# Performance work log

Measured on AMD Instinct MI355X. Metric: run time of the kernel, lower is better.

## Reference

```python
import jax, jax.numpy as jnp
import numpy as np

MODEL_DIM = 2048
HEAD_DIM = 64
STATE_DIM = 128
EXPAND = 2
CHUNK = 64
INNER = EXPAND * MODEL_DIM          # 4096
NHEADS = INNER // HEAD_DIM          # 64
IN_PROJ = INNER + 2 * STATE_DIM + NHEADS  # 4416
B_SZ = 2
SEQ = 4096


def segsum(x):
    """Stable segment sum: x (..., T) -> (..., T, T) with -inf above diagonal."""
    T = x.shape[-1]
    mask_strict = jnp.tril(jnp.ones((T, T), dtype=bool), -1)
    # element [d, e] = x[d] on strictly-lower triangle, 0 elsewhere
    xt = jnp.where(mask_strict, x[..., :, None], 0.0)
    seg = jnp.cumsum(xt, axis=-2)
    mask = jnp.tril(jnp.ones((T, T), dtype=bool), 0)
    return jnp.where(mask, seg, -jnp.inf)


def ssd(x, A, B, C, chunk):
    """Mamba-2 SSD. x:(b,L,h,p), A:(b,L,h), B/C:(b,L,n) shared over heads."""
    b, L, h, p = x.shape
    n = B.shape[-1]
    c = L // chunk
    x = x.reshape(b, c, chunk, h, p)
    A = A.reshape(b, c, chunk, h).transpose(0, 3, 1, 2)  # (b,h,c,l)
    B = B.reshape(b, c, chunk, n)
    C = C.reshape(b, c, chunk, n)

    A_cs = jnp.cumsum(A, axis=-1)                        # (b,h,c,l)
    Lm = jnp.exp(segsum(A))                              # (b,h,c,l,l)
    # 1. diagonal (intra-chunk) output
    Y_diag = jnp.einsum('bcln,bcsn,bhcls,bcshp->bclhp', C, B, Lm, x)
    # 2. per-chunk states
    decay_states = jnp.exp(A_cs[..., -1:] - A_cs)        # (b,h,c,l)
    states = jnp.einsum('bcln,bhcl,bclhp->bchpn', B, decay_states, x)
    states = jnp.concatenate([jnp.zeros_like(states[:, :1]), states], axis=1)
    # 3. inter-chunk recurrence
    A_chunk = jnp.pad(A_cs[..., -1], ((0, 0), (0, 0), (1, 0)))   # (b,h,c+1)
    decay_chunk = jnp.exp(segsum(A_chunk))               # (b,h,c+1,c+1)
    new_states = jnp.einsum('bhzc,bchpn->bzhpn', decay_chunk, states)
    states_prev, final_state = new_states[:, :-1], new_states[:, -1]
    # 4. state -> output
    Y_off = jnp.einsum('bcln,bchpn,bhcl->bclhp', C, states_prev, jnp.exp(A_cs))
    Y = (Y_diag + Y_off).reshape(b, L, h, p)
    return Y, final_state


def setup_inputs() -> dict:
    key = jax.random.key(0)
    ks = jax.random.split(key, 6)
    u = jax.random.normal(ks[0], (B_SZ, SEQ, MODEL_DIM), jnp.float32)
    W_in = jax.random.normal(ks[1], (IN_PROJ, MODEL_DIM), jnp.float32) * 0.02
    b_in = jnp.zeros((IN_PROJ,), jnp.float32)
    W_out = jax.random.normal(ks[2], (MODEL_DIM, INNER), jnp.float32) * 0.02
    b_out = jnp.zeros((MODEL_DIM,), jnp.float32)
    # A_log = log(uniform(1, 16)) per Mamba-2 init
    A_log = jnp.log(jax.random.uniform(ks[3], (NHEADS,), jnp.float32, 1.0, 16.0))
    # dt_bias = inv-softplus of dt ~ loguniform(1e-3, 1e-1)
    dt = jnp.exp(jax.random.uniform(ks[4], (NHEADS,), jnp.float32)
                 * (np.log(0.1) - np.log(0.001)) + np.log(0.001))
    dt = jnp.clip(dt, 1e-4, None)
    dt_bias = dt + jnp.log(-jnp.expm1(-dt))
    return {'u': u, 'W_in': W_in, 'b_in': b_in, 'W_out': W_out,
            'b_out': b_out, 'A_log': A_log, 'dt_bias': dt_bias}


def reference(u, W_in, b_in, W_out, b_out, A_log, dt_bias):
    xBCdt = u @ W_in.T + b_in                       # (b, L, IN_PROJ)
    x, Bm, Cm, dt = jnp.split(
        xBCdt, [INNER, INNER + STATE_DIM, INNER + 2 * STATE_DIM], axis=-1)
    A = -jnp.exp(A_log)                             # (h,)
    dt = jax.nn.softplus(dt + dt_bias)              # (b, L, h)
    x = x.reshape(B_SZ, SEQ, NHEADS, HEAD_DIM)
    y, final_state = ssd(x * dt[..., None], A * dt, Bm, Cm, CHUNK)
    y = y.reshape(B_SZ, SEQ, INNER)
    y = y @ W_out.T + b_out
    return y, final_state
```

## Files before the change

kernel.cpp:

```cpp
#include <hip/hip_runtime.h>
#include <hip/hip_bf16.h>

typedef __hip_bfloat16 bf16;
typedef __attribute__((ext_vector_type(8))) short short8;
typedef __attribute__((ext_vector_type(4))) float f32x4;

#define MODEL_DIM 2048
#define INNER     4096
#define NHEADS    64
#define HEAD_DIM  64
#define STATE_DIM 128
#define IN_PROJ   4416
#define BSZ       2
#define SEQ       4096
#define CHUNKL    64
#define NTOK      (BSZ*SEQ)
#define NCHUNK    (SEQ/CHUNKL)

#define WAITV0() asm volatile("s_waitcnt vmcnt(0)" ::: "memory")
#define BAR()    __builtin_amdgcn_s_barrier()
#define SCHEDB() __builtin_amdgcn_sched_barrier(0)
#define WAITLG(N) do { asm volatile("s_waitcnt lgkmcnt(" #N ")" ::: "memory"); SCHEDB(); } while (0)

#define SWZ(x) ((x) ^ ((((x) >> 7) & 7) << 4))

static __device__ __forceinline__ void gload_lds16(const bf16* g, bf16* l) {
  __builtin_amdgcn_global_load_lds((const __attribute__((address_space(1))) void*)g,
                                   (__attribute__((address_space(3))) void*)l, 16, 0, 0);
}

static __device__ __forceinline__ unsigned lds_u32(const void* p) {
  return (unsigned)(unsigned long long)(const __attribute__((address_space(3))) char*)p;
}

static __device__ __forceinline__ short8 ds_read128(unsigned addr) {
  short8 r;
  asm volatile("ds_read_b128 %0, %1" : "=v"(r) : "v"(addr));
  return r;
}

static __device__ __forceinline__ void stage_unit(const bf16* __restrict__ P, int K,
                                                  int blockRow, int kt,
                                                  char* region, int unit, int t) {
  int o = unit * 8192 + (t << 4);
  int lb = SWZ(o);
  int row = lb >> 7, colb = lb & 127;
  gload_lds16(P + (size_t)(blockRow + row) * K + kt + (colb >> 1), (bf16*)(region + o));
}

#define MFMA_BLK(MLO, MHI, NLO, NHI)                                                    \
  __builtin_amdgcn_s_setprio(1);                                                       \
  _Pragma("unroll") for (int mf = (MLO); mf < (MHI); ++mf)                             \
    _Pragma("unroll") for (int nf = (NLO); nf < (NHI); ++nf)                           \
      _Pragma("unroll") for (int ks = 0; ks < 2; ++ks)                                 \
        acc[mf][nf] = __builtin_amdgcn_mfma_f32_16x16x32_bf16(a[mf][ks], b[nf][ks],    \
                                                              acc[mf][nf], 0, 0, 0);  \
  __builtin_amdgcn_s_setprio(0);

template<int BN>
static __device__ __forceinline__ void gemm_core1(
    const bf16* __restrict__ Ag, const bf16* __restrict__ Bg,
    int K, int NT, int bm, int bn, char* lds, f32x4 (&acc)[8][BN / 64]) {
  constexpr int NR = BN / 64;
  constexpr int BB = 32768 + NR * 8192;
  const int t = threadIdx.x;
  const int lane = t & 63;
  const int wid = t >> 6, wm = wid >> 2, wn = wid & 3;
  const unsigned x16 = (unsigned)(lane & 7) << 4;
  const unsigned kb0 = (unsigned)(lane >> 4) << 4;
  const unsigned ldsB = lds_u32(lds);
  const unsigned aRow0 = (unsigned)(wm * 128 + (lane & 15)) * 128;
  const unsigned bRow0 = (unsigned)(wn * (BN / 4) + (lane & 15)) * 128;

#pragma unroll
  for (int u = 0; u < 4; ++u) stage_unit(Ag, K, bm, 0, lds, u, t);
#pragma unroll
  for (int u = 0; u < NR; ++u) stage_unit(Bg, K, bn, 0, lds + 32768, u, t);
  WAITV0();
  BAR();

  int cur = 0;
  for (int tt = 0; tt < NT; ++tt) {
    char* oth = lds + (cur ^ 1) * BB;
    const unsigned aB = ldsB + (unsigned)(cur * BB);
    const unsigned bB = aB + 32768;
    const bool st = (tt + 1 < NT);

    if (st) {
      const int kt1 = (tt + 1) * 64;
#pragma unroll
      for (int u = 0; u < 4; ++u) stage_unit(Ag, K, bm, kt1, oth, u, t);
#pragma unroll
      for (int u = 0; u < NR; ++u) stage_unit(Bg, K, bn, kt1, oth + 32768, u, t);
    }

    short8 a[8][2], b[NR][2];
#pragma unroll
    for (int mf = 0; mf < 4; ++mf)
#pragma unroll
      for (int ks = 0; ks < 2; ++ks)
        a[mf][ks] = ds_read128(aB + aRow0 + mf * 2048 + (((unsigned)(ks * 64) + kb0) ^ x16));
#pragma unroll
    for (int nf = 0; nf < 2; ++nf)
#pragma unroll
      for (int ks = 0; ks < 2; ++ks)
        b[nf][ks] = ds_read128(bB + bRow0 + nf * 2048 + (((unsigned)(ks * 64) + kb0) ^ x16));
#pragma unroll
    for (int mf = 4; mf < 8; ++mf)
#pragma unroll
      for (int ks = 0; ks < 2; ++ks)
        a[mf][ks] = ds_read128(aB + aRow0 + mf * 2048 + (((unsigned)(ks * 64) + kb0) ^ x16));
#pragma unroll
    for (int nf = 2; nf < NR; ++nf)
#pragma unroll
      for (int ks = 0; ks < 2; ++ks)
        b[nf][ks] = ds_read128(bB + bRow0 + nf * 2048 + (((unsigned)(ks * 64) + kb0) ^ x16));

    if constexpr (NR == 4) WAITLG(12); else WAITLG(10);
    MFMA_BLK(0, 4, 0, 2);
    if constexpr (NR == 4) WAITLG(4);  else WAITLG(2);
    MFMA_BLK(4, 8, 0, 2);
    WAITLG(0);
    MFMA_BLK(0, 8, 2, NR);

    if (st) WAITV0();
    BAR();
    cur ^= 1;
  }
}

__global__ __launch_bounds__(512, 2)
void gemm_in256(const bf16* __restrict__ A, const bf16* __restrict__ Bw,
                const float* __restrict__ bias, bf16* __restrict__ x_bf,
                bf16* __restrict__ B_bf, bf16* __restrict__ C_bf, float* __restrict__ dtraw) {
  __shared__ char lds[2 * (32768 + 3 * 8192)];
  int nwg = gridDim.x, bid = blockIdx.x;
  int cpx = nwg >> 3;
  int sb = (bid & 7) * cpx + (bid >> 3);
  int bx = sb % (IN_PROJ / 192), by = sb / (IN_PROJ / 192);
  int bm = by * 256, bn = bx * 192;
  f32x4 acc[8][3] = {};
  gemm_core1<192>(A, Bw, MODEL_DIM, MODEL_DIM / 64, bm, bn, lds, acc);
  const int lane = threadIdx.x & 63, wid = threadIdx.x >> 6;
  const int wm = wid >> 2, wn = wid & 3;
#pragma unroll
  for (int mf = 0; mf < 8; ++mf)
#pragma unroll
    for (int nf = 0; nf < 3; ++nf)
#pragma unroll
      for (int r = 0; r < 4; ++r) {
        int row = bm + wm * 128 + mf * 16 + (lane >> 4) * 4 + r;
        int col = bn + wn * 48 + nf * 16 + (lane & 15);
        float v = acc[mf][nf][r] + bias[col];
        if (col < 4096)       x_bf[(size_t)row * 4096 + col]         = __float2bfloat16(v);
        else if (col < 4224)  B_bf[(size_t)row * 128 + (col - 4096)] = __float2bfloat16(v);
        else if (col < 4352)  C_bf[(size_t)row * 128 + (col - 4224)] = __float2bfloat16(v);
        else                  dtraw[(size_t)row * 64 + (col - 4352)] = v;
      }
}

__global__ __launch_bounds__(512, 2)
void gemm_out256(const bf16* __restrict__ A, const bf16* __restrict__ Bw,
                 const float* __restrict__ bias, float* __restrict__ C) {
  __shared__ char lds[2 * (32768 + 4 * 8192)];
  int nwg = gridDim.x, bid = blockIdx.x;
  int cpx = nwg >> 3;
  int sb = (bid & 7) * cpx + (bid >> 3);
  int bx = sb % (MODEL_DIM / 256), by = sb / (MODEL_DIM / 256);
  int bm = by * 256, bn = bx * 256;
  f32x4 acc[8][4] = {};
  gemm_core1<256>(A, Bw, INNER, INNER / 64, bm, bn, lds, acc);
  const int lane = threadIdx.x & 63, wid = threadIdx.x >> 6;
  const int wm = wid >> 2, wn = wid & 3;
#pragma unroll
  for (int mf = 0; mf < 8; ++mf)
#pragma unroll
    for (int nf = 0; nf < 4; ++nf)
#pragma unroll
      for (int r = 0; r < 4; ++r) {
        int row = bm + wm * 128 + mf * 16 + (lane >> 4) * 4 + r;
        int col = bn + wn * 64 + nf * 16 + (lane & 15);
        C[(size_t)row * MODEL_DIM + col] = acc[mf][nf][r] + bias[col];
      }
}

__global__ __launch_bounds__(256) void conv_f32_to_bf16(const float* __restrict__ src,
                                                        bf16* __restrict__ dst, int n4) {
  int i = blockIdx.x * 256 + threadIdx.x;
  if (i >= n4) return;
  float4 v = *(const float4*)(src + (size_t)i * 4);
  bf16* d = dst + (size_t)i * 4;
  d[0] = __float2bfloat16(v.x); d[1] = __float2bfloat16(v.y);
  d[2] = __float2bfloat16(v.z); d[3] = __float2bfloat16(v.w);
}

__global__ __launch_bounds__(256)
void prep_small(const float* __restrict__ dtraw, const float* __restrict__ A_log,
                const float* __restrict__ dt_bias, float* __restrict__ dts,
                float* __restrict__ a_dt) {
  int i = blockIdx.x * 256 + threadIdx.x;
  int h = i & 63;
  float z = dtraw[i] + dt_bias[h];
  float dt = (z > 20.f) ? z : log1pf(expf(z));
  dts[i] = dt;
  a_dt[i] = -expf(A_log[h]) * dt;
}

__global__ __launch_bounds__(256)
void g_pre_kernel(const bf16* __restrict__ B_bf, const bf16* __restrict__ C_bf,
                  float* __restrict__ G_g) {
  __shared__ bf16 Cs[64 * 128];
  __shared__ bf16 Bs[64 * 128];
  int blk = blockIdx.x;
  int t = threadIdx.x, lane = t & 63, wid = t >> 6;
  int tokBase = (blk >> 6) * SEQ + (blk & 63) * 64;

#pragma unroll
  for (int i = 0; i < 4; ++i) {
    int chunk = t + i * 256;
    int l = chunk >> 4, n0 = (chunk & 15) * 8;
    *(short8*)(Cs + l * 128 + n0) = *(const short8*)(C_bf + (size_t)(tokBase + l) * 128 + n0);
    *(short8*)(Bs + l * 128 + n0) = *(const short8*)(B_bf + (size_t)(tokBase + l) * 128 + n0);
  }
  __syncthreads();

  int lBase = (wid >> 1) * 32, sBase = (wid & 1) * 32;
  f32x4 g[2][2] = {};
#pragma unroll
  for (int ks = 0; ks < 4; ++ks) {
    short8 a[2], bb[2];
#pragma unroll
    for (int mi = 0; mi < 2; ++mi)
      a[mi] = *(const short8*)(Cs + (lBase + mi * 16 + (lane & 15)) * 128 + ks * 32 + (lane >> 4) * 8);
#pragma unroll
    for (int ni = 0; ni < 2; ++ni)
      bb[ni] = *(const short8*)(Bs + (sBase + ni * 16 + (lane & 15)) * 128 + ks * 32 + (lane >> 4) * 8);
#pragma unroll
    for (int mi = 0; mi < 2; ++mi)
#pragma unroll
      for (int ni = 0; ni < 2; ++ni)
        g[mi][ni] = __builtin_amdgcn_mfma_f32_16x16x32_bf16(a[mi], bb[ni], g[mi][ni], 0, 0, 0);
  }
  float* Gd = G_g + (size_t)blk * 4096;
#pragma unroll
  for (int mi = 0; mi < 2; ++mi)
#pragma unroll
    for (int ni = 0; ni < 2; ++ni)
#pragma unroll
      for (int r = 0; r < 4; ++r) {
        int row = lBase + mi * 16 + (lane >> 4) * 4 + r;
        int col = sBase + ni * 16 + (lane & 15);
        Gd[row * 64 + col] = g[mi][ni][r];
      }
}

#define LP 72
__global__ __launch_bounds__(256)
void ssd_fused_kernel(const bf16* __restrict__ x_bf, const bf16* __restrict__ B_bf,
                      const float* __restrict__ dts_g, const float* __restrict__ a_dt,
                      float* __restrict__ acs_g, bf16* __restrict__ states_g,
                      float* __restrict__ out_fs) {
  __shared__ bf16 xT[2][32 * LP];
  __shared__ bf16 BT[2][128 * LP];
  __shared__ float sc_s[2][64];
  __shared__ float dfac_s[4];
  int blk = blockIdx.x;
  int pg = blk & 1, h = (blk >> 1) & 63, b = blk >> 7;
  int t = threadIdx.x, lane = t & 63, w = t >> 6;
  int lx = t >> 2, sx = t & 3;

  f32x4 S4[4] = {};
  short8 rxC, rBC[4], rxN, rBN[4];
  float raN = 0.f, rdtN = 0.f;

  {
    int tb = b * SEQ;
    rxC = *(const short8*)(x_bf + (size_t)(tb + lx) * 4096 + h * 64 + pg * 32 + sx * 8);
#pragma unroll
    for (int k = 0; k < 4; ++k)
      rBC[k] = *(const short8*)(B_bf + (size_t)(tb + lx) * 128 + sx * 32 + k * 8);
    if (t < 64) {
      float ra0 = a_dt[(size_t)(tb + t) * 64 + h];
      float rdt0 = dts_g[(size_t)(tb + t) * 64 + h];
      float v = ra0;
#pragma unroll
      for (int d = 1; d < 64; d <<= 1) { float o = __shfl_up(v, d); if (t >= d) v += o; }
      float a63 = __shfl(v, 63);
      if (pg == 0) acs_g[(((size_t)(b * 64 + 0)) * 64 + h) * 64 + t] = v;
      sc_s[0][t] = rdt0 * expf(a63 - v);
      if (t == 0) dfac_s[0] = expf(a63);
    }
    int tb1 = tb + 64;
    rxN = *(const short8*)(x_bf + (size_t)(tb1 + lx) * 4096 + h * 64 + pg * 32 + sx * 8);
#pragma unroll
    for (int k = 0; k < 4; ++k)
      rBN[k] = *(const short8*)(B_bf + (size_t)(tb1 + lx) * 128 + sx * 32 + k * 8);
    if (t < 64) {
      raN = a_dt[(size_t)(tb1 + t) * 64 + h];
      rdtN = dts_g[(size_t)(tb1 + t) * 64 + h];
    }
  }
  __syncthreads();

  for (int c = 0; c < 64; ++c) {
    int c2 = (c < 62) ? c + 2 : 63;
    int tb2 = b * SEQ + c2 * 64;
    short8 rxI = *(const short8*)(x_bf + (size_t)(tb2 + lx) * 4096 + h * 64 + pg * 32 + sx * 8);
    short8 rBI[4];
#pragma unroll
    for (int k = 0; k < 4; ++k)
      rBI[k] = *(const short8*)(B_bf + (size_t)(tb2 + lx) * 128 + sx * 32 + k * 8);
    float raI = 0.f, rdtI = 0.f;
    if (t < 64) {
      raI = a_dt[(size_t)(tb2 + t) * 64 + h];
      rdtI = dts_g[(size_t)(tb2 + t) * 64 + h];
    }

    int bufc = c & 1;
    {
      float s_l = sc_s[bufc][lx];
      const bf16* pv = (const bf16*)&rxC;
#pragma unroll
      for (int j = 0; j < 8; ++j)
        xT[bufc][(sx * 8 + j) * LP + lx] = __float2bfloat16(__bfloat162float(pv[j]) * s_l);
#pragma unroll
      for (int k = 0; k < 4; ++k) {
        const bf16* pb = (const bf16*)&rBC[k];
        int n0 = sx * 32 + k * 8;
#pragma unroll
        for (int j = 0; j < 8; ++j) BT[bufc][(n0 + j) * LP + lx] = pb[j];
      }
    }
    if (t < 64) {
      float v = raN;
#pragma unroll
      for (int d = 1; d < 64; d <<= 1) { float o = __shfl_up(v, d); if (t >= d) v += o; }
      float a63 = __shfl(v, 63);
      if (c + 1 < 64 && pg == 0)
        acs_g[(((size_t)(b * 64 + c + 1)) * 64 + h) * 64 + t] = v;
      sc_s[(c + 1) & 1][t] = rdtN * expf(a63 - v);
      if (t == 0) dfac_s[(c + 1) & 3] = expf(a63);
    }
    __syncthreads();

    float dfac = dfac_s[c & 3];
    int ps = (w >> 1) * 16, nb = (w & 1) * 64;
    f32x4 acc[4] = {};
    short8 af[2];
#pragma unroll
    for (int ks = 0; ks < 2; ++ks)
      af[ks] = *(const short8*)(&xT[bufc][(ps + (lane & 15)) * LP + ks * 32 + (lane >> 4) * 8]);
#pragma unroll
    for (int nf = 0; nf < 4; ++nf)
#pragma unroll
      for (int ks = 0; ks < 2; ++ks) {
        short8 bf_ = *(const short8*)(&BT[bufc][(nb + nf * 16 + (lane & 15)) * LP + ks * 32 + (lane >> 4) * 8]);
        acc[nf] = __builtin_amdgcn_mfma_f32_16x16x32_bf16(af[ks], bf_, acc[nf], 0, 0, 0);
      }
    size_t sbase = ((size_t)((b * 64 + c) * 64 + h)) * 8192;
#pragma unroll
    for (int nf = 0; nf < 4; ++nf)
#pragma unroll
      for (int r = 0; r < 4; ++r) {
        int p = pg * 32 + ps + (lane >> 4) * 4 + r;
        int n = nb + nf * 16 + (lane & 15);
        states_g[sbase + (size_t)p * 128 + n] = __float2bfloat16(S4[nf][r]);
        S4[nf][r] = dfac * S4[nf][r] + acc[nf][r];
      }

    rxC = rxN; rxN = rxI;
#pragma unroll
    for (int k = 0; k < 4; ++k) { rBC[k] = rBN[k]; rBN[k] = rBI[k]; }
    raN = raI; rdtN = rdtI;
  }

  size_t ob = ((size_t)(b * 64 + h)) * 8192;
  int ps = (w >> 1) * 16, nb = (w & 1) * 64;
#pragma unroll
  for (int nf = 0; nf < 4; ++nf)
#pragma unroll
    for (int r = 0; r < 4; ++r) {
      int p = pg * 32 + ps + (lane >> 4) * 4 + r;
      int n = nb + nf * 16 + (lane & 15);
      out_fs[ob + (size_t)p * 128 + n] = S4[nf][r];
    }
}

__global__ __launch_bounds__(256)
void ssd_out_kernel(bf16* __restrict__ x_bf, const bf16* __restrict__ C_bf,
                    const float* __restrict__ dts, const float* __restrict__ acs_g,
                    const bf16* __restrict__ states_g, const float* __restrict__ G_g) {
  __shared__ bf16 Cs[64 * 128];
  __shared__ bf16 Ms[64 * 64];
  __shared__ bf16 xT[64 * 64];
  __shared__ bf16 Sp[64 * 128];
  __shared__ float acs_s[2][64];
  int blk = blockIdx.x;
  int hg = blk & 15, c = (blk >> 4) & 63, b = blk >> 10;
  int t = threadIdx.x, lane = t & 63, wid = t >> 6;
  int tokBase = b * SEQ + c * 64;

  int lBase = (wid >> 1) * 32, sBase = (wid & 1) * 32;
  const float* Gd = G_g + ((size_t)(b * 64 + c)) * 4096;
  float gv[2][2][4];
#pragma unroll
  for (int mi = 0; mi < 2; ++mi)
#pragma unroll
    for (int ni = 0; ni < 2; ++ni)
#pragma unroll
      for (int r = 0; r < 4; ++r)
        gv[mi][ni][r] = Gd[(lBase + mi * 16 + (lane >> 4) * 4 + r) * 64 +
                           sBase + ni * 16 + (lane & 15)];

#pragma unroll
  for (int i = 0; i < 4; ++i) {
    int chunk = t + i * 256;
    int l = chunk >> 4, n0 = (chunk & 15) * 8;
    *(short8*)(Cs + l * 128 + n0) = *(const short8*)(C_bf + (size_t)(tokBase + l) * 128 + n0);
  }

  for (int hi = 0; hi < 4; ++hi) {
    int h = hg * 4 + hi;
    size_t sbase = ((size_t)((b * 64 + c) * 64 + h)) * 8192;

    if (t < 64) acs_s[hi & 1][t] = acs_g[(((size_t)(b * 64 + c)) * 64 + h) * 64 + t];
#pragma unroll
    for (int i = 0; i < 2; ++i) {
      int chunk = t + i * 256;
      int l = chunk >> 3, p0 = (chunk & 7) * 8;
      float dtv = dts[(size_t)(tokBase + l) * 64 + h];
      short8 vv = *(const short8*)(x_bf + (size_t)(tokBase + l) * 4096 + h * 64 + p0);
      const bf16* pv = (const bf16*)&vv;
#pragma unroll
      for (int j = 0; j < 8; ++j)
        xT[(p0 + j) * 64 + l] = __float2bfloat16(__bfloat162float(pv[j]) * dtv);
    }
#pragma unroll
    for (int i = 0; i < 4; ++i) {
      int chunk = t + i * 256;
      *(short8*)(Sp + chunk * 8) = *(const short8*)(states_g + sbase + chunk * 8);
    }
    __syncthreads();

#pragma unroll
    for (int mi = 0; mi < 2; ++mi)
#pragma unroll
      for (int ni = 0; ni < 2; ++ni)
#pragma unroll
        for (int r = 0; r < 4; ++r) {
          int row = lBase + mi * 16 + (lane >> 4) * 4 + r;
          int col = sBase + ni * 16 + (lane & 15);
          float lm = (row >= col) ? expf(acs_s[hi & 1][row] - acs_s[hi & 1][col]) : 0.f;
          Ms[row * 64 + col] = __float2bfloat16(gv[mi][ni][r] * lm);
        }
    __syncthreads();

    int pBase = (wid & 1) * 32;
    f32x4 yd[2][2] = {}, yo[2][2] = {};
#pragma unroll
    for (int ks = 0; ks < 2; ++ks) {
      short8 a[2], bb[2];
#pragma unroll
      for (int mi = 0; mi < 2; ++mi)
        a[mi] = *(const short8*)(Ms + (lBase + mi * 16 + (lane & 15)) * 64 + ks * 32 + (lane >> 4) * 8);
#pragma unroll
      for (int ni = 0; ni < 2; ++ni)
        bb[ni] = *(const short8*)(xT + (pBase + ni * 16 + (lane & 15)) * 64 + ks * 32 + (lane >> 4) * 8);
#pragma unroll
      for (int mi = 0; mi < 2; ++mi)
#pragma unroll
        for (int ni = 0; ni < 2; ++ni)
          yd[mi][ni] = __builtin_amdgcn_mfma_f32_16x16x32_bf16(a[mi], bb[ni], yd[mi][ni], 0, 0, 0);
    }
#pragma unroll
    for (int ks = 0; ks < 4; ++ks) {
      short8 a[2], bb[2];
#pragma unroll
      for (int mi = 0; mi < 2; ++mi)
        a[mi] = *(const short8*)(Cs + (lBase + mi * 16 + (lane & 15)) * 128 + ks * 32 + (lane >> 4) * 8);
#pragma unroll
      for (int ni = 0; ni < 2; ++ni)
        bb[ni] = *(const short8*)(Sp + (pBase + ni * 16 + (lane & 15)) * 128 + ks * 32 + (lane >> 4) * 8);
#pragma unroll
      for (int mi = 0; mi < 2; ++mi)
#pragma unroll
        for (int ni = 0; ni < 2; ++ni)
          yo[mi][ni] = __builtin_amdgcn_mfma_f32_16x16x32_bf16(a[mi], bb[ni], yo[mi][ni], 0, 0, 0);
    }
    __syncthreads();

#pragma unroll
    for (int mi = 0; mi < 2; ++mi)
#pragma unroll
      for (int ni = 0; ni < 2; ++ni)
#pragma unroll
        for (int r = 0; r < 4; ++r) {
          int lr = lBase + mi * 16 + (lane >> 4) * 4 + r;
          int p = pBase + ni * 16 + (lane & 15);
          float val = yd[mi][ni][r] + expf(acs_s[hi & 1][lr]) * yo[mi][ni][r];
          x_bf[(size_t)(tokBase + lr) * 4096 + h * 64 + p] = __float2bfloat16(val);
        }
  }
}

extern "C" void kernel_launch(void* const* d_in, const int* in_sizes, int n_in,
                              void* d_out, int out_size, void* d_ws, size_t ws_size,
                              hipStream_t stream) {
  const float* u       = (const float*)d_in[0];
  const float* W_in    = (const float*)d_in[1];
  const float* b_in    = (const float*)d_in[2];
  const float* W_out   = (const float*)d_in[3];
  const float* b_out   = (const float*)d_in[4];
  const float* A_log   = (const float*)d_in[5];
  const float* dt_bias = (const float*)d_in[6];

  float* y_out  = (float*)d_out;
  float* fs_out = y_out + (size_t)NTOK * MODEL_DIM;

  char* ws = (char*)d_ws;
  size_t off = 0;
  auto alloc = [&](size_t bytes) { char* p = ws + off; off += (bytes + 255) & ~255ull; return p; };
  bf16*  wout_bf = (bf16*) alloc((size_t)MODEL_DIM * INNER * 2);
  bf16*  x_bf    = (bf16*) alloc((size_t)NTOK * INNER * 2);
  bf16*  B_bf    = (bf16*) alloc((size_t)NTOK * STATE_DIM * 2);
  bf16*  C_bf    = (bf16*) alloc((size_t)NTOK * STATE_DIM * 2);
  float* dtraw   = (float*)alloc((size_t)NTOK * NHEADS * 4);
  float* dts     = (float*)alloc((size_t)NTOK * NHEADS * 4);
  float* a_dt    = (float*)alloc((size_t)NTOK * NHEADS * 4);
  float* acs     = (float*)alloc((size_t)BSZ * NCHUNK * NHEADS * 64 * 4);
  float* gbuf    = (float*)alloc((size_t)BSZ * NCHUNK * 4096 * 4);
  char*  Q       = alloc((size_t)BSZ * NCHUNK * NHEADS * 64 * 128 * 2);
  bf16*  states  = (bf16*)Q;
  bf16*  u_bf    = (bf16*)Q;
  bf16*  win_bf  = u_bf + (size_t)NTOK * MODEL_DIM;
  (void)ws_size; (void)off; (void)in_sizes; (void)n_in; (void)out_size;

  conv_f32_to_bf16<<<dim3(16384), dim3(256), 0, stream>>>(u, u_bf, NTOK * MODEL_DIM / 4);
  conv_f32_to_bf16<<<dim3(IN_PROJ * MODEL_DIM / 1024), dim3(256), 0, stream>>>(
      W_in, win_bf, IN_PROJ * MODEL_DIM / 4);
  conv_f32_to_bf16<<<dim3(8192), dim3(256), 0, stream>>>(W_out, wout_bf, MODEL_DIM * INNER / 4);

  gemm_in256<<<dim3((NTOK / 256) * (IN_PROJ / 192)), dim3(512), 0, stream>>>(
      u_bf, win_bf, b_in, x_bf, B_bf, C_bf, dtraw);

  prep_small<<<dim3(NTOK * NHEADS / 256), dim3(256), 0, stream>>>(dtraw, A_log, dt_bias, dts, a_dt);

  g_pre_kernel<<<dim3(BSZ * NCHUNK), dim3(256), 0, stream>>>(B_bf, C_bf, gbuf);

  ssd_fused_kernel<<<dim3(BSZ * NHEADS * 2), dim3(256), 0, stream>>>(
      x_bf, B_bf, dts, a_dt, acs, states, fs_out);

  ssd_out_kernel<<<dim3(BSZ * NCHUNK * 16), dim3(256), 0, stream>>>(
      x_bf, C_bf, dts, acs, states, gbuf);

  gemm_out256<<<dim3((MODEL_DIM / 256) * (NTOK / 256)), dim3(512), 0, stream>>>(
      x_bf, wout_bf, b_out, y_out);
}
```

Before: 487.7 us.

## Fuse SSD chunk-state recurrence and chunk output into one kernel

```diff
diff --git a/kernel.cpp b/kernel.cpp
--- a/kernel.cpp
+++ b/kernel.cpp
@@ -254,51 +254,62 @@
       }
 }
 
-#define LP 72
+#define LPX 72
+#define LPC 136
 __global__ __launch_bounds__(256)
-void ssd_fused_kernel(const bf16* __restrict__ x_bf, const bf16* __restrict__ B_bf,
-                      const float* __restrict__ dts_g, const float* __restrict__ a_dt,
-                      float* __restrict__ acs_g, bf16* __restrict__ states_g,
-                      float* __restrict__ out_fs) {
-  __shared__ bf16 xT[2][32 * LP];
-  __shared__ bf16 BT[2][128 * LP];
-  __shared__ float sc_s[2][64];
+void ssd_mega_kernel(bf16* __restrict__ x_bf, const bf16* __restrict__ B_bf,
+                     const bf16* __restrict__ C_bf, const float* __restrict__ dts_g,
+                     const float* __restrict__ a_dt, const float* __restrict__ G_g,
+                     float* __restrict__ out_fs) {
+  __shared__ bf16 xT[2][32 * LPX];
+  __shared__ bf16 BT[2][128 * LPX];
+  __shared__ bf16 Cs[2][64 * LPC];
+  __shared__ bf16 Sp[32 * LPC];
+  __shared__ bf16 Ms[64 * LPX];
+  __shared__ float acv_s[4][64];
+  __shared__ float scB_s[2][64];
+  __shared__ float dtl_s[2][64];
   __shared__ float dfac_s[4];
+
   int blk = blockIdx.x;
   int pg = blk & 1, h = (blk >> 1) & 63, b = blk >> 7;
   int t = threadIdx.x, lane = t & 63, w = t >> 6;
   int lx = t >> 2, sx = t & 3;
-
-  f32x4 S4[4] = {};
-  short8 rxC, rBC[4], rxN, rBN[4];
+  int nq = w * 32;
+  int lq = w * 16;
+  int lBase = (w >> 1) * 32, sBase = (w & 1) * 32;
+
+  f32x4 S4[2][2] = {};
+
+  short8 rxC, rxN, rBC[4], rBN[4], rCC[4], rCN[4];
   float raN = 0.f, rdtN = 0.f;
 
   {
     int tb = b * SEQ;
     rxC = *(const short8*)(x_bf + (size_t)(tb + lx) * 4096 + h * 64 + pg * 32 + sx * 8);
 #pragma unroll
-    for (int k = 0; k < 4; ++k)
+    for (int k = 0; k < 4; ++k) {
       rBC[k] = *(const short8*)(B_bf + (size_t)(tb + lx) * 128 + sx * 32 + k * 8);
+      rCC[k] = *(const short8*)(C_bf + (size_t)(tb + lx) * 128 + sx * 32 + k * 8);
+    }
     if (t < 64) {
       float ra0 = a_dt[(size_t)(tb + t) * 64 + h];
-      float rdt0 = dts_g[(size_t)(tb + t) * 64 + h];
+      float rd0 = dts_g[(size_t)(tb + t) * 64 + h];
       float v = ra0;
 #pragma unroll
       for (int d = 1; d < 64; d <<= 1) { float o = __shfl_up(v, d); if (t >= d) v += o; }
       float a63 = __shfl(v, 63);
-      if (pg == 0) acs_g[(((size_t)(b * 64 + 0)) * 64 + h) * 64 + t] = v;
-      sc_s[0][t] = rdt0 * expf(a63 - v);
+      acv_s[0][t] = v; scB_s[0][t] = expf(a63 - v); dtl_s[0][t] = rd0;
       if (t == 0) dfac_s[0] = expf(a63);
     }
     int tb1 = tb + 64;
     rxN = *(const short8*)(x_bf + (size_t)(tb1 + lx) * 4096 + h * 64 + pg * 32 + sx * 8);
 #pragma unroll
-    for (int k = 0; k < 4; ++k)
+    for (int k = 0; k < 4; ++k) {
       rBN[k] = *(const short8*)(B_bf + (size_t)(tb1 + lx) * 128 + sx * 32 + k * 8);
-    if (t < 64) {
-      raN = a_dt[(size_t)(tb1 + t) * 64 + h];
-      rdtN = dts_g[(size_t)(tb1 + t) * 64 + h];
-    }
+      rCN[k] = *(const short8*)(C_bf + (size_t)(tb1 + lx) * 128 + sx * 32 + k * 8);
+    }
+    if (t < 64) { raN = a_dt[(size_t)(tb1 + t) * 64 + h]; rdtN = dts_g[(size_t)(tb1 + t) * 64 + h]; }
   }
   __syncthreads();
 
@@ -306,29 +317,41 @@
     int c2 = (c < 62) ? c + 2 : 63;
     int tb2 = b * SEQ + c2 * 64;
     short8 rxI = *(const short8*)(x_bf + (size_t)(tb2 + lx) * 4096 + h * 64 + pg * 32 + sx * 8);
-    short8 rBI[4];
-#pragma unroll
-    for (int k = 0; k < 4; ++k)
+    short8 rBI[4], rCI[4];
+#pragma unroll
+    for (int k = 0; k < 4; ++k) {
       rBI[k] = *(const short8*)(B_bf + (size_t)(tb2 + lx) * 128 + sx * 32 + k * 8);
+      rCI[k] = *(const short8*)(C_bf + (size_t)(tb2 + lx) * 128 + sx * 32 + k * 8);
+    }
     float raI = 0.f, rdtI = 0.f;
-    if (t < 64) {
-      raI = a_dt[(size_t)(tb2 + t) * 64 + h];
-      rdtI = dts_g[(size_t)(tb2 + t) * 64 + h];
-    }
+    if (t < 64) { raI = a_dt[(size_t)(tb2 + t) * 64 + h]; rdtI = dts_g[(size_t)(tb2 + t) * 64 + h]; }
+    const float* Gd = G_g + ((size_t)(b * 64 + c)) * 4096;
+    float gv[2][2][4];
+#pragma unroll
+    for (int mi = 0; mi < 2; ++mi)
+#pragma unroll
+      for (int ni = 0; ni < 2; ++ni)
+#pragma unroll
+        for (int r = 0; r < 4; ++r)
+          gv[mi][ni][r] = Gd[(lBase + mi * 16 + (lane >> 4) * 4 + r) * 64 +
+                             sBase + ni * 16 + (lane & 15)];
 
     int bufc = c & 1;
     {
-      float s_l = sc_s[bufc][lx];
+      float dtv = dtl_s[bufc][lx];
       const bf16* pv = (const bf16*)&rxC;
 #pragma unroll
       for (int j = 0; j < 8; ++j)
-        xT[bufc][(sx * 8 + j) * LP + lx] = __float2bfloat16(__bfloat162float(pv[j]) * s_l);
+        xT[bufc][(sx * 8 + j) * LPX + lx] = __float2bfloat16(__bfloat162float(pv[j]) * dtv);
+      float decB = scB_s[bufc][lx];
 #pragma unroll
       for (int k = 0; k < 4; ++k) {
         const bf16* pb = (const bf16*)&rBC[k];
         int n0 = sx * 32 + k * 8;
 #pragma unroll
-        for (int j = 0; j < 8; ++j) BT[bufc][(n0 + j) * LP + lx] = pb[j];
+        for (int j = 0; j < 8; ++j)
+          BT[bufc][(n0 + j) * LPX + lx] = __float2bfloat16(__bfloat162float(pb[j]) * decB);
+        *(short8*)(&Cs[bufc][lx * LPC + sx * 32 + k * 8]) = rCC[k];
       }
     }
     if (t < 64) {
@@ -336,112 +359,43 @@
 #pragma unroll
       for (int d = 1; d < 64; d <<= 1) { float o = __shfl_up(v, d); if (t >= d) v += o; }
       float a63 = __shfl(v, 63);
-      if (c + 1 < 64 && pg == 0)
-        acs_g[(((size_t)(b * 64 + c + 1)) * 64 + h) * 64 + t] = v;
-      sc_s[(c + 1) & 1][t] = rdtN * expf(a63 - v);
+      acv_s[(c + 1) & 3][t] = v;
+      scB_s[(c + 1) & 1][t] = expf(a63 - v);
+      dtl_s[(c + 1) & 1][t] = rdtN;
       if (t == 0) dfac_s[(c + 1) & 3] = expf(a63);
     }
     __syncthreads();
 
-    float dfac = dfac_s[c & 3];
-    int ps = (w >> 1) * 16, nb = (w & 1) * 64;
-    f32x4 acc[4] = {};
-    short8 af[2];
-#pragma unroll
-    for (int ks = 0; ks < 2; ++ks)
-      af[ks] = *(const short8*)(&xT[bufc][(ps + (lane & 15)) * LP + ks * 32 + (lane >> 4) * 8]);
-#pragma unroll
-    for (int nf = 0; nf < 4; ++nf)
-#pragma unroll
-      for (int ks = 0; ks < 2; ++ks) {
-        short8 bf_ = *(const short8*)(&BT[bufc][(nb + nf * 16 + (lane & 15)) * LP + ks * 32 + (lane >> 4) * 8]);
-        acc[nf] = __builtin_amdgcn_mfma_f32_16x16x32_bf16(af[ks], bf_, acc[nf], 0, 0, 0);
-      }
-    size_t sbase = ((size_t)((b * 64 + c) * 64 + h)) * 8192;
-#pragma unroll
-    for (int nf = 0; nf < 4; ++nf)
-#pragma unroll
-      for (int r = 0; r < 4; ++r) {
-        int p = pg * 32 + ps + (lane >> 4) * 4 + r;
-        int n = nb + nf * 16 + (lane & 15);
-        states_g[sbase + (size_t)p * 128 + n] = __float2bfloat16(S4[nf][r]);
-        S4[nf][r] = dfac * S4[nf][r] + acc[nf][r];
-      }
-
-    rxC = rxN; rxN = rxI;
-#pragma unroll
-    for (int k = 0; k < 4; ++k) { rBC[k] = rBN[k]; rBN[k] = rBI[k]; }
-    raN = raI; rdtN = rdtI;
-  }
-
-  size_t ob = ((size_t)(b * 64 + h)) * 8192;
-  int ps = (w >> 1) * 16, nb = (w & 1) * 64;
-#pragma unroll
-  for (int nf = 0; nf < 4; ++nf)
-#pragma unroll
-    for (int r = 0; r < 4; ++r) {
-      int p = pg * 32 + ps + (lane >> 4) * 4 + r;
-      int n = nb + nf * 16 + (lane & 15);
-      out_fs[ob + (size_t)p * 128 + n] = S4[nf][r];
-    }
-}
-
-__global__ __launch_bounds__(256)
-void ssd_out_kernel(bf16* __restrict__ x_bf, const bf16* __restrict__ C_bf,
-                    const float* __restrict__ dts, const float* __restrict__ acs_g,
-                    const bf16* __restrict__ states_g, const float* __restrict__ G_g) {
-  __shared__ bf16 Cs[64 * 128];
-  __shared__ bf16 Ms[64 * 64];
-  __shared__ bf16 xT[64 * 64];
-  __shared__ bf16 Sp[64 * 128];
-  __shared__ float acs_s[2][64];
-  int blk = blockIdx.x;
-  int hg = blk & 15, c = (blk >> 4) & 63, b = blk >> 10;
-  int t = threadIdx.x, lane = t & 63, wid = t >> 6;
-  int tokBase = b * SEQ + c * 64;
-
-  int lBase = (wid >> 1) * 32, sBase = (wid & 1) * 32;
-  const float* Gd = G_g + ((size_t)(b * 64 + c)) * 4096;
-  float gv[2][2][4];
-#pragma unroll
-  for (int mi = 0; mi < 2; ++mi)
-#pragma unroll
-    for (int ni = 0; ni < 2; ++ni)
-#pragma unroll
-      for (int r = 0; r < 4; ++r)
-        gv[mi][ni][r] = Gd[(lBase + mi * 16 + (lane >> 4) * 4 + r) * 64 +
-                           sBase + ni * 16 + (lane & 15)];
-
-#pragma unroll
-  for (int i = 0; i < 4; ++i) {
-    int chunk = t + i * 256;
-    int l = chunk >> 4, n0 = (chunk & 15) * 8;
-    *(short8*)(Cs + l * 128 + n0) = *(const short8*)(C_bf + (size_t)(tokBase + l) * 128 + n0);
-  }
-
-  for (int hi = 0; hi < 4; ++hi) {
-    int h = hg * 4 + hi;
-    size_t sbase = ((size_t)((b * 64 + c) * 64 + h)) * 8192;
-
-    if (t < 64) acs_s[hi & 1][t] = acs_g[(((size_t)(b * 64 + c)) * 64 + h) * 64 + t];
-#pragma unroll
-    for (int i = 0; i < 2; ++i) {
-      int chunk = t + i * 256;
-      int l = chunk >> 3, p0 = (chunk & 7) * 8;
-      float dtv = dts[(size_t)(tokBase + l) * 64 + h];
-      short8 vv = *(const short8*)(x_bf + (size_t)(tokBase + l) * 4096 + h * 64 + p0);
-      const bf16* pv = (const bf16*)&vv;
-#pragma unroll
-      for (int j = 0; j < 8; ++j)
-        xT[(p0 + j) * 64 + l] = __float2bfloat16(__bfloat162float(pv[j]) * dtv);
-    }
-#pragma unroll
-    for (int i = 0; i < 4; ++i) {
-      int chunk = t + i * 256;
-      *(short8*)(Sp + chunk * 8) = *(const short8*)(states_g + sbase + chunk * 8);
-    }
-    __syncthreads();
-
+    {
+      f32x4 cs[2][2] = {};
+      short8 axf[2][2];
+#pragma unroll
+      for (int pf = 0; pf < 2; ++pf)
+#pragma unroll
+        for (int ks = 0; ks < 2; ++ks)
+          axf[pf][ks] = *(const short8*)(&xT[bufc][(pf * 16 + (lane & 15)) * LPX + ks * 32 + (lane >> 4) * 8]);
+#pragma unroll
+      for (int nf = 0; nf < 2; ++nf)
+#pragma unroll
+        for (int ks = 0; ks < 2; ++ks) {
+          short8 bbf = *(const short8*)(&BT[bufc][(nq + nf * 16 + (lane & 15)) * LPX + ks * 32 + (lane >> 4) * 8]);
+#pragma unroll
+          for (int pf = 0; pf < 2; ++pf)
+            cs[pf][nf] = __builtin_amdgcn_mfma_f32_16x16x32_bf16(axf[pf][ks], bbf, cs[pf][nf], 0, 0, 0);
+        }
+      float dfac = dfac_s[c & 3];
+#pragma unroll
+      for (int pf = 0; pf < 2; ++pf)
+#pragma unroll
+        for (int nf = 0; nf < 2; ++nf)
+#pragma unroll
+          for (int r = 0; r < 4; ++r) {
+            int pp = pf * 16 + (lane >> 4) * 4 + r;
+            int n = nq + nf * 16 + (lane & 15);
+            Sp[pp * LPC + n] = __float2bfloat16(S4[pf][nf][r]);
+            S4[pf][nf][r] = dfac * S4[pf][nf][r] + cs[pf][nf][r];
+          }
+    }
 #pragma unroll
     for (int mi = 0; mi < 2; ++mi)
 #pragma unroll
@@ -450,57 +404,61 @@
         for (int r = 0; r < 4; ++r) {
           int row = lBase + mi * 16 + (lane >> 4) * 4 + r;
           int col = sBase + ni * 16 + (lane & 15);
-          float lm = (row >= col) ? expf(acs_s[hi & 1][row] - acs_s[hi & 1][col]) : 0.f;
-          Ms[row * 64 + col] = __float2bfloat16(gv[mi][ni][r] * lm);
+          float lm = (row >= col) ? expf(acv_s[c & 3][row] - acv_s[c & 3][col]) : 0.f;
+          Ms[row * LPX + col] = __float2bfloat16(gv[mi][ni][r] * lm);
         }
     __syncthreads();
 
-    int pBase = (wid & 1) * 32;
-    f32x4 yd[2][2] = {}, yo[2][2] = {};
-#pragma unroll
-    for (int ks = 0; ks < 2; ++ks) {
-      short8 a[2], bb[2];
-#pragma unroll
-      for (int mi = 0; mi < 2; ++mi)
-        a[mi] = *(const short8*)(Ms + (lBase + mi * 16 + (lane & 15)) * 64 + ks * 32 + (lane >> 4) * 8);
-#pragma unroll
-      for (int ni = 0; ni < 2; ++ni)
-        bb[ni] = *(const short8*)(xT + (pBase + ni * 16 + (lane & 15)) * 64 + ks * 32 + (lane >> 4) * 8);
-#pragma unroll
-      for (int mi = 0; mi < 2; ++mi)
-#pragma unroll
-        for (int ni = 0; ni < 2; ++ni)
-          yd[mi][ni] = __builtin_amdgcn_mfma_f32_16x16x32_bf16(a[mi], bb[ni], yd[mi][ni], 0, 0, 0);
-    }
-#pragma unroll
-    for (int ks = 0; ks < 4; ++ks) {
-      short8 a[2], bb[2];
-#pragma unroll
-      for (int mi = 0; mi < 2; ++mi)
-        a[mi] = *(const short8*)(Cs + (lBase + mi * 16 + (lane & 15)) * 128 + ks * 32 + (lane >> 4) * 8);
-#pragma unroll
-      for (int ni = 0; ni < 2; ++ni)
-        bb[ni] = *(const short8*)(Sp + (pBase + ni * 16 + (lane & 15)) * 128 + ks * 32 + (lane >> 4) * 8);
-#pragma unroll
-      for (int mi = 0; mi < 2; ++mi)
-#pragma unroll
-        for (int ni = 0; ni < 2; ++ni)
-          yo[mi][ni] = __builtin_amdgcn_mfma_f32_16x16x32_bf16(a[mi], bb[ni], yo[mi][ni], 0, 0, 0);
-    }
-    __syncthreads();
-
-#pragma unroll
-    for (int mi = 0; mi < 2; ++mi)
-#pragma unroll
-      for (int ni = 0; ni < 2; ++ni)
+    {
+      f32x4 yd[2] = {}, yo[2] = {};
+#pragma unroll
+      for (int ks = 0; ks < 2; ++ks) {
+        short8 am = *(const short8*)(&Ms[(lq + (lane & 15)) * LPX + ks * 32 + (lane >> 4) * 8]);
+#pragma unroll
+        for (int pf = 0; pf < 2; ++pf) {
+          short8 bx = *(const short8*)(&xT[bufc][(pf * 16 + (lane & 15)) * LPX + ks * 32 + (lane >> 4) * 8]);
+          yd[pf] = __builtin_amdgcn_mfma_f32_16x16x32_bf16(am, bx, yd[pf], 0, 0, 0);
+        }
+      }
+#pragma unroll
+      for (int ks = 0; ks < 4; ++ks) {
+        short8 ac = *(const short8*)(&Cs[bufc][(lq + (lane & 15)) * LPC + ks * 32 + (lane >> 4) * 8]);
+#pragma unroll
+        for (int pf = 0; pf < 2; ++pf) {
+          short8 bs = *(const short8*)(&Sp[(pf * 16 + (lane & 15)) * LPC + ks * 32 + (lane >> 4) * 8]);
+          yo[pf] = __builtin_amdgcn_mfma_f32_16x16x32_bf16(ac, bs, yo[pf], 0, 0, 0);
+        }
+      }
+      int tokBase = b * SEQ + c * 64;
+#pragma unroll
+      for (int pf = 0; pf < 2; ++pf)
 #pragma unroll
         for (int r = 0; r < 4; ++r) {
-          int lr = lBase + mi * 16 + (lane >> 4) * 4 + r;
-          int p = pBase + ni * 16 + (lane & 15);
-          float val = yd[mi][ni][r] + expf(acs_s[hi & 1][lr]) * yo[mi][ni][r];
-          x_bf[(size_t)(tokBase + lr) * 4096 + h * 64 + p] = __float2bfloat16(val);
+          int l = lq + (lane >> 4) * 4 + r;
+          float ev = expf(acv_s[c & 3][l]);
+          int p = pg * 32 + pf * 16 + (lane & 15);
+          x_bf[(size_t)(tokBase + l) * 4096 + h * 64 + p] =
+              __float2bfloat16(yd[pf][r] + ev * yo[pf][r]);
         }
+    }
+
+    rxC = rxN; rxN = rxI;
+#pragma unroll
+    for (int k = 0; k < 4; ++k) { rBC[k] = rBN[k]; rBN[k] = rBI[k]; rCC[k] = rCN[k]; rCN[k] = rCI[k]; }
+    raN = raI; rdtN = rdtI;
   }
+
+  size_t ob = ((size_t)(b * 64 + h)) * 8192;
+#pragma unroll
+  for (int pf = 0; pf < 2; ++pf)
+#pragma unroll
+    for (int nf = 0; nf < 2; ++nf)
+#pragma unroll
+      for (int r = 0; r < 4; ++r) {
+        int p = pg * 32 + pf * 16 + (lane >> 4) * 4 + r;
+        int n = nq + nf * 16 + (lane & 15);
+        out_fs[ob + (size_t)p * 128 + n] = S4[pf][nf][r];
+      }
 }
 
 extern "C" void kernel_launch(void* const* d_in, const int* in_sizes, int n_in,
@@ -527,12 +485,9 @@
   float* dtraw   = (float*)alloc((size_t)NTOK * NHEADS * 4);
   float* dts     = (float*)alloc((size_t)NTOK * NHEADS * 4);
   float* a_dt    = (float*)alloc((size_t)NTOK * NHEADS * 4);
-  float* acs     = (float*)alloc((size_t)BSZ * NCHUNK * NHEADS * 64 * 4);
   float* gbuf    = (float*)alloc((size_t)BSZ * NCHUNK * 4096 * 4);
-  char*  Q       = alloc((size_t)BSZ * NCHUNK * NHEADS * 64 * 128 * 2);
-  bf16*  states  = (bf16*)Q;
-  bf16*  u_bf    = (bf16*)Q;
-  bf16*  win_bf  = u_bf + (size_t)NTOK * MODEL_DIM;
+  bf16*  u_bf    = (bf16*) alloc((size_t)NTOK * MODEL_DIM * 2);
+  bf16*  win_bf  = (bf16*) alloc((size_t)IN_PROJ * MODEL_DIM * 2);
   (void)ws_size; (void)off; (void)in_sizes; (void)n_in; (void)out_size;
 
   conv_f32_to_bf16<<<dim3(16384), dim3(256), 0, stream>>>(u, u_bf, NTOK * MODEL_DIM / 4);
@@ -547,11 +502,8 @@
 
   g_pre_kernel<<<dim3(BSZ * NCHUNK), dim3(256), 0, stream>>>(B_bf, C_bf, gbuf);
 
-  ssd_fused_kernel<<<dim3(BSZ * NHEADS * 2), dim3(256), 0, stream>>>(
-      x_bf, B_bf, dts, a_dt, acs, states, fs_out);
-
-  ssd_out_kernel<<<dim3(BSZ * NCHUNK * 16), dim3(256), 0, stream>>>(
-      x_bf, C_bf, dts, acs, states, gbuf);
+  ssd_mega_kernel<<<dim3(BSZ * NHEADS * 2), dim3(256), 0, stream>>>(
+      x_bf, B_bf, C_bf, dts, a_dt, gbuf, fs_out);
 
   gemm_out256<<<dim3((MODEL_DIM / 256) * (NTOK / 256)), dim3(512), 0, stream>>>(
       x_bf, wout_bf, b_out, y_out);
```

After: 578.8 us. +18.7%, slower.
